# Performance work log

Measured on AMD Instinct MI355X. Metric: run time of the kernel, lower is better.

The kernel has to match this reference:

```python
import jax, jax.numpy as jnp
import numpy as np

P, F, FR = 288, 7, 12      # time slots per day, days per week, sampling frequency scale
CHEB_K = 2
HID = 64


def _ste(time_index, SE, W_se, b_se, T_tod, T_dow):
    """Spatio-temporal embedding: learned spatial embedding projected to et_dim,
    plus time-of-day and day-of-week temporal embeddings. -> [B, N, et]"""
    t = time_index * FR
    tod = T_tod[t % P]                 # [B, et]
    dow = T_dow[(t // P) % F]          # [B, et]
    se = SE @ W_se + b_se              # [N, et]
    return se[None, :, :] + (tod + dow)[:, None, :]


def _avwgcn(x, STE, R, SC, Wpool, bpool):
    """Adaptive-vertex-weight graph conv (AGCRN-style) with dynamic STE-driven
    adjacency blended with dynamic relation R and static correlation SC.
    x: [B,N,Cin], STE: [B,N,et], R: [B,N,N], SC: [N,N]."""
    A = jax.nn.softmax(
        jax.nn.relu(jnp.einsum('bnd,bmd->bnm', STE, STE)) + R + SC[None], axis=-1)
    # Chebyshev polynomial supports applied to x (T0 = I handled implicitly)
    xs = [x, jnp.einsum('bnm,bmc->bnc', A, x)]
    for _ in range(CHEB_K - 2):
        xs.append(2.0 * jnp.einsum('bnm,bmc->bnc', A, xs[-1]) - xs[-2])
    x_g = jnp.stack(xs, axis=2)                        # [B,N,K,Cin]
    # per-node adaptive weights: W_n = STE @ Wpool; contracted without
    # materializing the [B,N,K,Cin,Cout] tensor
    g = jnp.einsum('bnki,dkio->bndo', x_g, Wpool)      # [B,N,et,Cout]
    out = jnp.einsum('bndo,bnd->bno', g, STE) + jnp.einsum('bnd,do->bno', STE, bpool)
    return out


def setup_inputs() -> dict:
    key = jax.random.key(0)
    ks = jax.random.split(key, 12)
    B, N, Din, et, es = 32, 1024, 1, 16, 16
    std = 0.1
    return {
        "x": jax.random.normal(ks[0], (B, N, Din), jnp.float32),
        "R": jax.random.normal(ks[1], (B, N, N), jnp.float32) * std,
        "state": jax.random.normal(ks[2], (B, N, HID), jnp.float32),
        "SC": jax.random.normal(ks[3], (N, N), jnp.float32) * std,
        "SE": jax.random.normal(ks[4], (N, es), jnp.float32),
        "W_se": jax.random.normal(ks[5], (es, et), jnp.float32) * std,
        "b_se": jnp.zeros((et,), jnp.float32),
        "T_tod": jax.random.normal(ks[6], (P, et), jnp.float32) * std,
        "T_dow": jax.random.normal(ks[7], (F, et), jnp.float32) * std,
        "W_gate": jax.random.normal(ks[8], (et, CHEB_K, Din + HID, 2 * HID), jnp.float32) * std,
        "b_gate": jnp.zeros((et, 2 * HID), jnp.float32),
        "W_upd": jax.random.normal(ks[9], (et, CHEB_K, Din + HID, HID), jnp.float32) * std,
        "b_upd": jnp.zeros((et, HID), jnp.float32),
        "time_index": jax.random.randint(ks[10], (B,), 0, P * F),
    }


def reference(x, R, state, SC, SE, W_se, b_se, T_tod, T_dow,
              W_gate, b_gate, W_upd, b_upd, time_index):
    STE = _ste(time_index, SE, W_se, b_se, T_tod, T_dow)       # [B,N,et]
    ins = jnp.concatenate([x, state], axis=-1)                 # [B,N,Din+H]
    z_r = jax.nn.sigmoid(_avwgcn(ins, STE, R, SC, W_gate, b_gate))
    z, r = jnp.split(z_r, 2, axis=-1)                          # each [B,N,H]
    cand = jnp.concatenate([x, z * state], axis=-1)
    hc = jnp.tanh(_avwgcn(cand, STE, R, SC, W_upd, b_upd))
    return r * state + (1.0 - r) * hc                          # [B,N,H]
```

## Files before the change

kernel.cpp:

```cpp
#include <hip/hip_runtime.h>
#include <math.h>

namespace {
constexpr int BB = 32;
constexpr int NN = 1024;
constexpr int ET = 16;
constexpr int HH = 64;
constexpr int CIN = 65;
constexpr int KI = 2*CIN;
constexpr int COG = 2*HH;
constexpr int COU = HH;
constexpr int PP = 288;
constexpr int FF = 7;
constexpr int FRQ = 12;
constexpr int XK = 160;

typedef __attribute__((ext_vector_type(4))) float f32x4;
typedef __attribute__((ext_vector_type(8))) short s16x8;
typedef unsigned long long ull;

__device__ __forceinline__ float bf2f(unsigned short u) {
    unsigned v = ((unsigned)u) << 16;
    return __builtin_bit_cast(float, v);
}
__device__ __forceinline__ unsigned short f2bf(float f) {
    unsigned u = __builtin_bit_cast(unsigned, f);
    u += 0x7fffu + ((u >> 16) & 1u);
    return (unsigned short)(u >> 16);
}
__device__ __forceinline__ float ldany(const float* p) { return *p; }
__device__ __forceinline__ float ldany(const unsigned short* p) { return bf2f(*p); }

__global__ void k_prep1(const float* __restrict__ SE, const float* __restrict__ Wse,
                        const float* __restrict__ bse, const float* __restrict__ Ttod,
                        const float* __restrict__ Tdow, const int* __restrict__ tidx,
                        float* __restrict__ se, float* __restrict__ tt) {
    int idx = blockIdx.x*blockDim.x + threadIdx.x;
    if (idx < NN*ET) {
        int n = idx / ET, d = idx % ET;
        float acc = bse[d];
        #pragma unroll
        for (int e = 0; e < ET; ++e) acc += SE[n*ET + e]*Wse[e*ET + d];
        se[idx] = acc;
    } else if (idx < NN*ET + BB*ET) {
        int r = idx - NN*ET;
        int b = r / ET, d = r % ET;
        int t = tidx[b]*FRQ;
        tt[r] = Ttod[(t % PP)*ET + d] + Tdow[((t/PP) % FF)*ET + d];
    }
}

__global__ void k_prep2bf(const float* __restrict__ se, const float* __restrict__ tt,
                          unsigned short* __restrict__ stebf) {
    int idx = blockIdx.x*blockDim.x + threadIdx.x;
    if (idx >= BB*NN*ET) return;
    int d = idx % ET;
    int n = (idx/ET) % NN;
    int b = idx/(ET*NN);
    stebf[idx] = f2bf(se[n*ET+d] + tt[b*ET+d]);
}

__global__ void k_prepWpt(const float* __restrict__ Wg, const float* __restrict__ Wu,
                          unsigned short* __restrict__ Wptg, unsigned short* __restrict__ Wptu) {
    int idx = blockIdx.x*blockDim.x + threadIdx.x;
    constexpr int NG2 = ET*COG*XK;
    constexpr int NU2 = ET*COU*XK;
    if (idx < NG2) {
        int d = idx/(COG*XK), r = idx%(COG*XK), o = r/XK, ki = r%XK;
        float v = (ki < KI) ? Wg[((size_t)d*KI + ki)*COG + o] : 0.f;
        Wptg[((size_t)d*COG + o)*XK + ki] = f2bf(v);
    } else if (idx < NG2 + NU2) {
        int j = idx - NG2;
        int d = j/(COU*XK), r = j%(COU*XK), o = r/XK, ki = r%XK;
        float v = (ki < KI) ? Wu[((size_t)d*KI + ki)*COU + o] : 0.f;
        Wptu[((size_t)d*COU + o)*XK + ki] = f2bf(v);
    }
}

template<typename T>
__global__ void k_pack(const float* __restrict__ x, const T* __restrict__ sv,
                       unsigned short* __restrict__ xgbf) {
    int idx = blockIdx.x*blockDim.x + threadIdx.x;
    if (idx >= BB*NN*(XK/2)) return;
    int row = idx/(XK/2), c = idx%(XK/2);
    if (c < 32) {
        int k0 = 2*c;
        float v0 = (k0 == 0) ? x[row] : ldany(sv + (size_t)row*HH + k0 - 1);
        float v1 = ldany(sv + (size_t)row*HH + k0);
        ((unsigned*)xgbf)[(size_t)row*(XK/2) + c] = ((unsigned)f2bf(v1) << 16) | f2bf(v0);
    } else if (c == 32) {
        xgbf[(size_t)row*XK + 64] = f2bf(ldany(sv + (size_t)row*HH + 63));
    } else if (c >= 65) {
        ((unsigned*)xgbf)[(size_t)row*(XK/2) + c] = 0;
    }
}

template<typename T>
__global__ void k_cvtVt(const T* __restrict__ V, unsigned short* __restrict__ vt) {
    int idx = blockIdx.x*blockDim.x + threadIdx.x;
    if (idx >= BB*128*64) return;
    int och = idx & 63, mb = (idx >> 6) & 127, b = idx >> 13;
    const T* src = V + ((size_t)b*NN + mb*8)*HH + och;
    float v0=ldany(src), v1=ldany(src+HH), v2=ldany(src+2*HH), v3=ldany(src+3*HH);
    float v4=ldany(src+4*HH), v5=ldany(src+5*HH), v6=ldany(src+6*HH), v7=ldany(src+7*HH);
    ull lo = (ull)f2bf(v0) | ((ull)f2bf(v1)<<16) | ((ull)f2bf(v2)<<32) | ((ull)f2bf(v3)<<48);
    ull hi = (ull)f2bf(v4) | ((ull)f2bf(v5)<<16) | ((ull)f2bf(v6)<<32) | ((ull)f2bf(v7)<<48);
    ull* dst = (ull*)(vt + (size_t)idx*8);
    dst[0] = lo; dst[1] = hi;
}

constexpr int SSTR   = 1048;
constexpr int S_OFF  = 0;
constexpr int XV_OFF = 33536;
constexpr int MSH_OFF  = 37632;
constexpr int MSHC_OFF = 37888;
constexpr int LP_OFF   = 37952;
constexpr int AXP_OFF  = 38208;
constexpr int LSH_OFF  = 38464;
constexpr int SMEM_BYTES = 38528;

template<int PASS>
__global__ __launch_bounds__(256, 4) void k_attn(
    const unsigned short* __restrict__ stebf, const float* __restrict__ Rg,
    const float* __restrict__ SCg, const float* __restrict__ xg,
    const unsigned short* __restrict__ vt,
    float* __restrict__ Mr, float* __restrict__ Li,
    unsigned short* __restrict__ xgout)
{
    extern __shared__ char smem[];
    const int t = threadIdx.x, lane = t & 63, w = t >> 6;
    const int c15 = lane & 15, g = lane >> 4;
    const int strip = blockIdx.x, b = blockIdx.y;
    const size_t bN = (size_t)b * NN;
    const int r0 = strip * 16;

    float* Mshf  = (float*)(smem + MSH_OFF);
    float* MshCf = (float*)(smem + MSHC_OFF);
    float* Lpf   = (float*)(smem + LP_OFF);
    float* Axpf  = (float*)(smem + AXP_OFF);
    float* Lshf  = (float*)(smem + LSH_OFF);

    if (PASS == 1) {
        ((float4*)(smem + XV_OFF))[t] = ((const float4*)(xg + bN))[t];
    }

    {
        s16x8 af = {0,0,0,0,0,0,0,0};
        if (g < 2) af = *(const s16x8*)(stebf + (bN + r0 + c15)*ET + g*8);
        const float* Rb  = Rg  + (bN + r0 + g*4)*NN;
        const float* SCb = SCg + (size_t)(r0 + g*4)*NN;
        float mx0 = -INFINITY, mx1 = -INFINITY, mx2 = -INFINITY, mx3 = -INFINITY;
        float rc[4], scv[4];
        {
            int col = w*16 + c15;
            #pragma unroll
            for (int q = 0; q < 4; ++q) { rc[q] = Rb[(size_t)q*NN + col]; scv[q] = SCb[(size_t)q*NN + col]; }
        }
        for (int j = 0; j < 16; ++j) {
            int colB = j*64 + w*16 + c15;
            s16x8 bf = {0,0,0,0,0,0,0,0};
            if (g < 2) bf = *(const s16x8*)(stebf + (bN + colB)*ET + g*8);
            float rn[4] = {0.f,0.f,0.f,0.f}, sn[4] = {0.f,0.f,0.f,0.f};
            if (j < 15) {
                int col = colB + 64;
                #pragma unroll
                for (int q = 0; q < 4; ++q) { rn[q] = Rb[(size_t)q*NN + col]; sn[q] = SCb[(size_t)q*NN + col]; }
            }
            f32x4 zero = {0.f,0.f,0.f,0.f};
            f32x4 d = __builtin_amdgcn_mfma_f32_16x16x32_bf16(af, bf, zero, 0, 0, 0);
            #pragma unroll
            for (int q = 0; q < 4; ++q) {
                float s = fmaxf(d[q], 0.f) + rc[q] + scv[q];
                if (PASS == 1) {
                    if (q == 0) mx0 = fmaxf(mx0, s);
                    if (q == 1) mx1 = fmaxf(mx1, s);
                    if (q == 2) mx2 = fmaxf(mx2, s);
                    if (q == 3) mx3 = fmaxf(mx3, s);
                }
                int rowl = g*4 + q;
                *(unsigned short*)(smem + S_OFF + (unsigned)(rowl*SSTR + colB)*2u) = f2bf(s);
            }
            #pragma unroll
            for (int q = 0; q < 4; ++q) { rc[q] = rn[q]; scv[q] = sn[q]; }
        }
        if (PASS == 1) {
            float mxa[4] = {mx0, mx1, mx2, mx3};
            #pragma unroll
            for (int q = 0; q < 4; ++q) {
                float m = mxa[q];
                m = fmaxf(m, __shfl_xor(m, 1));
                m = fmaxf(m, __shfl_xor(m, 2));
                m = fmaxf(m, __shfl_xor(m, 4));
                m = fmaxf(m, __shfl_xor(m, 8));
                if (c15 == 0) Mshf[w*16 + g*4 + q] = m;
            }
        }
    }
    __syncthreads();

    if (PASS == 1) {
        if (t < 16) {
            float m = fmaxf(fmaxf(Mshf[t], Mshf[16+t]), fmaxf(Mshf[32+t], Mshf[48+t]));
            MshCf[t] = m;
            Mr[bN + r0 + t] = m;
        }
    } else {
        if (t < 16) MshCf[t] = Mr[bN + r0 + t];
        if (t >= 64 && t < 80) Lshf[t-64] = Li[bN + r0 + (t-64)];
    }
    __syncthreads();

    {
        const int rowl = c15;
        const float m = MshCf[rowl];
        float L = 0.f, ax = 0.f;
        for (int it = 0; it < 16; ++it) {
            int k = w*256 + it*16 + g*4;
            unsigned byteo = (unsigned)(rowl*SSTR + k)*2u;
            ull v = *(ull*)(smem + S_OFF + byteo);
            float s0 = bf2f((unsigned short)v);
            float s1 = bf2f((unsigned short)(v >> 16));
            float s2 = bf2f((unsigned short)(v >> 32));
            float s3 = bf2f((unsigned short)(v >> 48));
            float p0 = __expf(s0 - m), p1 = __expf(s1 - m);
            float p2 = __expf(s2 - m), p3 = __expf(s3 - m);
            if (PASS == 1) {
                float4 xq = *(const float4*)(smem + XV_OFF + k*4);
                L += (p0 + p1) + (p2 + p3);
                ax += p0*xq.x + p1*xq.y + p2*xq.z + p3*xq.w;
            }
            unsigned lo = ((unsigned)f2bf(p1) << 16) | f2bf(p0);
            unsigned hi = ((unsigned)f2bf(p3) << 16) | f2bf(p2);
            *(ull*)(smem + S_OFF + byteo) = ((ull)hi << 32) | lo;
        }
        if (PASS == 1) {
            L += __shfl_xor(L, 16); L += __shfl_xor(L, 32);
            ax += __shfl_xor(ax, 16); ax += __shfl_xor(ax, 32);
            if (g == 0) { Lpf[w*16 + rowl] = L; Axpf[w*16 + rowl] = ax; }
        }
    }
    __syncthreads();
    if (PASS == 1) {
        if (t < 16) {
            float Lt = Lpf[t] + Lpf[16+t] + Lpf[32+t] + Lpf[48+t];
            float li = 1.f / Lt;
            Lshf[t] = li;
            Li[bN + r0 + t] = li;
            xgout[(bN + r0 + t)*XK + 65] =
                f2bf((Axpf[t] + Axpf[16+t] + Axpf[32+t] + Axpf[48+t]) * li);
        }
        __syncthreads();
    }

    {
        f32x4 acc = {0.f,0.f,0.f,0.f};
        const unsigned short* vtb = vt + ((size_t)b*128*64 + (w*16 + c15))*8;
        #pragma unroll 4
        for (int j = 0; j < 16; ++j) {
            #pragma unroll
            for (int ks = 0; ks < 2; ++ks) {
                s16x8 a  = *(const s16x8*)(smem + S_OFF + (unsigned)(c15*SSTR + j*64 + ks*32 + g*8)*2u);
                s16x8 bv = *(const s16x8*)(vtb + (size_t)(j*8 + ks*4 + g)*512);
                acc = __builtin_amdgcn_mfma_f32_16x16x32_bf16(a, bv, acc, 0, 0, 0);
            }
        }
        #pragma unroll
        for (int q = 0; q < 4; ++q) {
            int rowl = g*4 + q;
            float li = Lshf[rowl];
            xgout[(bN + r0 + rowl)*XK + 66 + w*16 + c15] = f2bf(acc[q] * li);
        }
    }
}

template<int COUT, int EPI>
__global__ __launch_bounds__(256, 2) void k_apply(
    const unsigned short* __restrict__ Wpt, const float* __restrict__ bias,
    const unsigned short* __restrict__ stebf, const unsigned short* __restrict__ xgbf,
    const float* __restrict__ state, unsigned short* __restrict__ zsbf,
    unsigned short* __restrict__ rrbf, float* __restrict__ out)
{
    const int t = threadIdx.x, lane = t & 63, w = t >> 6;
    const int c15 = lane & 15, g = lane >> 4;
    const int n0 = blockIdx.x*32, b = blockIdx.y, oh = blockIdx.z;
    const int o = oh*64 + w*16 + c15;

    f32x4 acc[16][2];
    #pragma unroll
    for (int d = 0; d < 16; ++d) {
        acc[d][0] = (f32x4){0.f,0.f,0.f,0.f};
        acc[d][1] = (f32x4){0.f,0.f,0.f,0.f};
    }

    const unsigned short* Ar0 = xgbf + ((size_t)b*NN + n0 + c15)*XK + g*8;
    const unsigned short* Ar1 = Ar0 + (size_t)16*XK;
    const unsigned short* Bp  = Wpt + (size_t)o*XK + g*8;

    for (int ks = 0; ks < 5; ++ks) {
        s16x8 a0 = *(const s16x8*)(Ar0 + ks*32);
        s16x8 a1 = *(const s16x8*)(Ar1 + ks*32);
        #pragma unroll
        for (int d = 0; d < 16; ++d) {
            s16x8 bf = *(const s16x8*)(Bp + (size_t)d*COUT*XK + ks*32);
            acc[d][0] = __builtin_amdgcn_mfma_f32_16x16x32_bf16(a0, bf, acc[d][0], 0, 0, 0);
            acc[d][1] = __builtin_amdgcn_mfma_f32_16x16x32_bf16(a1, bf, acc[d][1], 0, 0, 0);
        }
    }

    float biasv[16];
    #pragma unroll
    for (int d = 0; d < 16; ++d) biasv[d] = bias[d*COUT + o];

    #pragma unroll
    for (int mt = 0; mt < 2; ++mt) {
        #pragma unroll
        for (int q = 0; q < 4; ++q) {
            int n = n0 + mt*16 + g*4 + q;
            size_t bn = (size_t)b*NN + n;
            const ull* sp = (const ull*)(stebf + bn*ET);
            float val = 0.f;
            #pragma unroll
            for (int dd = 0; dd < 4; ++dd) {
                ull sv4 = sp[dd];
                float s0 = bf2f((unsigned short)sv4);
                float s1 = bf2f((unsigned short)(sv4 >> 16));
                float s2 = bf2f((unsigned short)(sv4 >> 32));
                float s3 = bf2f((unsigned short)(sv4 >> 48));
                val += s0*(acc[dd*4+0][mt][q] + biasv[dd*4+0]);
                val += s1*(acc[dd*4+1][mt][q] + biasv[dd*4+1]);
                val += s2*(acc[dd*4+2][mt][q] + biasv[dd*4+2]);
                val += s3*(acc[dd*4+3][mt][q] + biasv[dd*4+3]);
            }
            if (EPI == 0) {
                float gv = 1.f/(1.f + __expf(-val));
                if (oh == 0) zsbf[bn*HH + o] = f2bf(gv * state[bn*HH + o]);
                else         rrbf[bn*HH + (o - 64)] = f2bf(gv);
            } else {
                float hc = tanhf(val);
                float rv = bf2f(rrbf[bn*HH + o]);
                out[bn*HH + o] = rv*state[bn*HH + o] + (1.f - rv)*hc;
            }
        }
    }
}

}

extern "C" void kernel_launch(void* const* d_in, const int* in_sizes, int n_in,
                              void* d_out, int out_size, void* d_ws, size_t ws_size,
                              hipStream_t stream) {
    const float* x     = (const float*)d_in[0];
    const float* R     = (const float*)d_in[1];
    const float* state = (const float*)d_in[2];
    const float* SC    = (const float*)d_in[3];
    const float* SE    = (const float*)d_in[4];
    const float* W_se  = (const float*)d_in[5];
    const float* b_se  = (const float*)d_in[6];
    const float* T_tod = (const float*)d_in[7];
    const float* T_dow = (const float*)d_in[8];
    const float* W_g   = (const float*)d_in[9];
    const float* b_g   = (const float*)d_in[10];
    const float* W_u   = (const float*)d_in[11];
    const float* b_u   = (const float*)d_in[12];
    const int*   tidx  = (const int*)d_in[13];
    float* out = (float*)d_out;
    float* ws = (float*)d_ws;

    float* se = ws;
    float* tt = se + 16384;
    float* Mr = tt + 512;
    float* Li = Mr + 32768;
    unsigned short* stebf = (unsigned short*)(Li + 32768);
    unsigned short* xgbf  = stebf + 524288;
    unsigned short* zsbf  = xgbf + 5242880;
    unsigned short* rrbf  = zsbf + 2097152;
    unsigned short* vt    = rrbf + 2097152;
    unsigned short* Wptg  = vt + 2097152;
    unsigned short* Wptu  = Wptg + 327680;

    k_prep1<<<66, 256, 0, stream>>>(SE, W_se, b_se, T_tod, T_dow, tidx, se, tt);
    k_prep2bf<<<2048, 256, 0, stream>>>(se, tt, stebf);
    k_prepWpt<<<1920, 256, 0, stream>>>(W_g, W_u, Wptg, Wptu);

    k_cvtVt<float><<<1024, 256, 0, stream>>>(state, vt);
    k_attn<1><<<dim3(64, 32), 256, SMEM_BYTES, stream>>>(
        stebf, R, SC, x, vt, Mr, Li, xgbf);
    k_pack<float><<<10240, 256, 0, stream>>>(x, state, xgbf);
    k_apply<COG, 0><<<dim3(32, 32, 2), 256, 0, stream>>>(
        Wptg, b_g, stebf, xgbf, state, zsbf, rrbf, nullptr);

    k_cvtVt<unsigned short><<<1024, 256, 0, stream>>>(zsbf, vt);
    k_attn<2><<<dim3(64, 32), 256, SMEM_BYTES, stream>>>(
        stebf, R, SC, x, vt, Mr, Li, xgbf);
    k_pack<unsigned short><<<10240, 256, 0, stream>>>(x, zsbf, xgbf);
    k_apply<COU, 1><<<dim3(32, 32, 1), 256, 0, stream>>>(
        Wptu, b_u, stebf, xgbf, state, zsbf, rrbf, out);
}
```

Measured before the change: 229.1 us.

## Fuse prep kernels, transpose score MFMA for row-contiguous loads, single-pass exp in pass two

Merges the STE and weight prep kernels into one launch, and merges the V transpose with the x/state packing so pass two's pack moves before its attention. In k_attn the score MFMA operands are swapped so each lane holds four contiguous columns of one row. That allows float4 loads of R and SC, packed bf16 stores via v_cvt_pk_bf16_f32, and a per-lane row max reduced with two shuffles. Pass two now applies exp with the stored row max while writing scores, dropping a sync and a full re-read of the shared-memory score tile. The cost is more kernel-body complexity and reliance on an inline-asm conversion instruction.

Result: no change. 233.6 us (+2.0%).

```diff
diff --git a/kernel.cpp b/kernel.cpp
--- a/kernel.cpp
+++ b/kernel.cpp
@@ -27,6 +27,11 @@
     unsigned u = __builtin_bit_cast(unsigned, f);
     u += 0x7fffu + ((u >> 16) & 1u);
     return (unsigned short)(u >> 16);
+}
+__device__ __forceinline__ unsigned cvtpk(float lo, float hi) {
+    unsigned r;
+    asm("v_cvt_pk_bf16_f32 %0, %1, %2" : "=v"(r) : "v"(lo), "v"(hi));
+    return r;
 }
 __device__ __forceinline__ float ldany(const float* p) { return *p; }
 __device__ __forceinline__ float ldany(const unsigned short* p) { return bf2f(*p); }
@@ -50,37 +55,49 @@
     }
 }
 
-__global__ void k_prep2bf(const float* __restrict__ se, const float* __restrict__ tt,
-                          unsigned short* __restrict__ stebf) {
+__global__ void k_prep2(const float* __restrict__ se, const float* __restrict__ tt,
+                        const float* __restrict__ Wg, const float* __restrict__ Wu,
+                        unsigned short* __restrict__ stebf,
+                        unsigned short* __restrict__ Wptg, unsigned short* __restrict__ Wptu) {
     int idx = blockIdx.x*blockDim.x + threadIdx.x;
-    if (idx >= BB*NN*ET) return;
-    int d = idx % ET;
-    int n = (idx/ET) % NN;
-    int b = idx/(ET*NN);
-    stebf[idx] = f2bf(se[n*ET+d] + tt[b*ET+d]);
-}
-
-__global__ void k_prepWpt(const float* __restrict__ Wg, const float* __restrict__ Wu,
-                          unsigned short* __restrict__ Wptg, unsigned short* __restrict__ Wptu) {
-    int idx = blockIdx.x*blockDim.x + threadIdx.x;
-    constexpr int NG2 = ET*COG*XK;
-    constexpr int NU2 = ET*COU*XK;
-    if (idx < NG2) {
+    if (idx < BB*NN*ET) {
+        int d = idx % ET;
+        int n = (idx/ET) % NN;
+        int b = idx/(ET*NN);
+        stebf[idx] = f2bf(se[n*ET+d] + tt[b*ET+d]);
+        return;
+    }
+    idx -= BB*NN*ET;
+    if (idx < ET*COG*XK) {
         int d = idx/(COG*XK), r = idx%(COG*XK), o = r/XK, ki = r%XK;
         float v = (ki < KI) ? Wg[((size_t)d*KI + ki)*COG + o] : 0.f;
         Wptg[((size_t)d*COG + o)*XK + ki] = f2bf(v);
-    } else if (idx < NG2 + NU2) {
-        int j = idx - NG2;
-        int d = j/(COU*XK), r = j%(COU*XK), o = r/XK, ki = r%XK;
+        return;
+    }
+    idx -= ET*COG*XK;
+    if (idx < ET*COU*XK) {
+        int d = idx/(COU*XK), r = idx%(COU*XK), o = r/XK, ki = r%XK;
         float v = (ki < KI) ? Wu[((size_t)d*KI + ki)*COU + o] : 0.f;
         Wptu[((size_t)d*COU + o)*XK + ki] = f2bf(v);
     }
 }
 
 template<typename T>
-__global__ void k_pack(const float* __restrict__ x, const T* __restrict__ sv,
-                       unsigned short* __restrict__ xgbf) {
+__global__ void k_vin(const float* __restrict__ x, const T* __restrict__ sv,
+                      unsigned short* __restrict__ xgbf, unsigned short* __restrict__ vt) {
     int idx = blockIdx.x*blockDim.x + threadIdx.x;
+    if (idx < BB*128*64) {
+        int och = idx & 63, mb = (idx >> 6) & 127, b = idx >> 13;
+        const T* src = sv + ((size_t)b*NN + mb*8)*HH + och;
+        float v0=ldany(src), v1=ldany(src+HH), v2=ldany(src+2*HH), v3=ldany(src+3*HH);
+        float v4=ldany(src+4*HH), v5=ldany(src+5*HH), v6=ldany(src+6*HH), v7=ldany(src+7*HH);
+        ull lo = (ull)f2bf(v0) | ((ull)f2bf(v1)<<16) | ((ull)f2bf(v2)<<32) | ((ull)f2bf(v3)<<48);
+        ull hi = (ull)f2bf(v4) | ((ull)f2bf(v5)<<16) | ((ull)f2bf(v6)<<32) | ((ull)f2bf(v7)<<48);
+        ull* dst = (ull*)(vt + (size_t)idx*8);
+        dst[0] = lo; dst[1] = hi;
+        return;
+    }
+    idx -= BB*128*64;
     if (idx >= BB*NN*(XK/2)) return;
     int row = idx/(XK/2), c = idx%(XK/2);
     if (c < 32) {
@@ -93,20 +110,6 @@
     } else if (c >= 65) {
         ((unsigned*)xgbf)[(size_t)row*(XK/2) + c] = 0;
     }
-}
-
-template<typename T>
-__global__ void k_cvtVt(const T* __restrict__ V, unsigned short* __restrict__ vt) {
-    int idx = blockIdx.x*blockDim.x + threadIdx.x;
-    if (idx >= BB*128*64) return;
-    int och = idx & 63, mb = (idx >> 6) & 127, b = idx >> 13;
-    const T* src = V + ((size_t)b*NN + mb*8)*HH + och;
-    float v0=ldany(src), v1=ldany(src+HH), v2=ldany(src+2*HH), v3=ldany(src+3*HH);
-    float v4=ldany(src+4*HH), v5=ldany(src+5*HH), v6=ldany(src+6*HH), v7=ldany(src+7*HH);
-    ull lo = (ull)f2bf(v0) | ((ull)f2bf(v1)<<16) | ((ull)f2bf(v2)<<32) | ((ull)f2bf(v3)<<48);
-    ull hi = (ull)f2bf(v4) | ((ull)f2bf(v5)<<16) | ((ull)f2bf(v6)<<32) | ((ull)f2bf(v7)<<48);
-    ull* dst = (ull*)(vt + (size_t)idx*8);
-    dst[0] = lo; dst[1] = hi;
 }
 
 constexpr int SSTR   = 1048;
@@ -142,113 +145,89 @@
 
     if (PASS == 1) {
         ((float4*)(smem + XV_OFF))[t] = ((const float4*)(xg + bN))[t];
-    }
-
+    } else {
+        if (t < 16) Lshf[t] = Li[bN + r0 + t];
+    }
+    float mp2 = 0.f;
+    if (PASS == 2) mp2 = Mr[bN + r0 + c15];
+
+    float mx = -INFINITY;
     {
-        s16x8 af = {0,0,0,0,0,0,0,0};
-        if (g < 2) af = *(const s16x8*)(stebf + (bN + r0 + c15)*ET + g*8);
-        const float* Rb  = Rg  + (bN + r0 + g*4)*NN;
-        const float* SCb = SCg + (size_t)(r0 + g*4)*NN;
-        float mx0 = -INFINITY, mx1 = -INFINITY, mx2 = -INFINITY, mx3 = -INFINITY;
-        float rc[4], scv[4];
-        {
-            int col = w*16 + c15;
-            #pragma unroll
-            for (int q = 0; q < 4; ++q) { rc[q] = Rb[(size_t)q*NN + col]; scv[q] = SCb[(size_t)q*NN + col]; }
-        }
+        s16x8 bfr = {0,0,0,0,0,0,0,0};
+        if (g < 2) bfr = *(const s16x8*)(stebf + (bN + r0 + c15)*ET + g*8);
+        const float* Rb  = Rg  + (bN + r0 + c15)*NN;
+        const float* SCb = SCg + (size_t)(r0 + c15)*NN;
+        const int colq = w*16 + g*4;
+        float4 rc = *(const float4*)(Rb + colq);
+        float4 sc = *(const float4*)(SCb + colq);
         for (int j = 0; j < 16; ++j) {
-            int colB = j*64 + w*16 + c15;
-            s16x8 bf = {0,0,0,0,0,0,0,0};
-            if (g < 2) bf = *(const s16x8*)(stebf + (bN + colB)*ET + g*8);
-            float rn[4] = {0.f,0.f,0.f,0.f}, sn[4] = {0.f,0.f,0.f,0.f};
+            s16x8 af = {0,0,0,0,0,0,0,0};
+            if (g < 2) af = *(const s16x8*)(stebf + (bN + j*64 + w*16 + c15)*ET + g*8);
+            float4 rn = {0,0,0,0}, sn = {0,0,0,0};
             if (j < 15) {
-                int col = colB + 64;
-                #pragma unroll
-                for (int q = 0; q < 4; ++q) { rn[q] = Rb[(size_t)q*NN + col]; sn[q] = SCb[(size_t)q*NN + col]; }
+                rn = *(const float4*)(Rb + colq + (j+1)*64);
+                sn = *(const float4*)(SCb + colq + (j+1)*64);
             }
             f32x4 zero = {0.f,0.f,0.f,0.f};
-            f32x4 d = __builtin_amdgcn_mfma_f32_16x16x32_bf16(af, bf, zero, 0, 0, 0);
-            #pragma unroll
-            for (int q = 0; q < 4; ++q) {
-                float s = fmaxf(d[q], 0.f) + rc[q] + scv[q];
-                if (PASS == 1) {
-                    if (q == 0) mx0 = fmaxf(mx0, s);
-                    if (q == 1) mx1 = fmaxf(mx1, s);
-                    if (q == 2) mx2 = fmaxf(mx2, s);
-                    if (q == 3) mx3 = fmaxf(mx3, s);
-                }
-                int rowl = g*4 + q;
-                *(unsigned short*)(smem + S_OFF + (unsigned)(rowl*SSTR + colB)*2u) = f2bf(s);
-            }
-            #pragma unroll
-            for (int q = 0; q < 4; ++q) { rc[q] = rn[q]; scv[q] = sn[q]; }
-        }
-        if (PASS == 1) {
-            float mxa[4] = {mx0, mx1, mx2, mx3};
-            #pragma unroll
-            for (int q = 0; q < 4; ++q) {
-                float m = mxa[q];
-                m = fmaxf(m, __shfl_xor(m, 1));
-                m = fmaxf(m, __shfl_xor(m, 2));
-                m = fmaxf(m, __shfl_xor(m, 4));
-                m = fmaxf(m, __shfl_xor(m, 8));
-                if (c15 == 0) Mshf[w*16 + g*4 + q] = m;
-            }
-        }
-    }
-    __syncthreads();
+            f32x4 d = __builtin_amdgcn_mfma_f32_16x16x32_bf16(af, bfr, zero, 0, 0, 0);
+            float s0 = fmaxf(d[0],0.f) + rc.x + sc.x;
+            float s1 = fmaxf(d[1],0.f) + rc.y + sc.y;
+            float s2 = fmaxf(d[2],0.f) + rc.z + sc.z;
+            float s3 = fmaxf(d[3],0.f) + rc.w + sc.w;
+            unsigned byteo = (unsigned)(c15*SSTR + j*64 + colq)*2u;
+            if (PASS == 1) {
+                mx = fmaxf(mx, fmaxf(fmaxf(s0,s1), fmaxf(s2,s3)));
+                *(ull*)(smem + S_OFF + byteo) = (ull)cvtpk(s0,s1) | ((ull)cvtpk(s2,s3) << 32);
+            } else {
+                float p0 = __expf(s0 - mp2), p1 = __expf(s1 - mp2);
+                float p2 = __expf(s2 - mp2), p3 = __expf(s3 - mp2);
+                *(ull*)(smem + S_OFF + byteo) = (ull)cvtpk(p0,p1) | ((ull)cvtpk(p2,p3) << 32);
+            }
+            rc = rn; sc = sn;
+        }
+    }
 
     if (PASS == 1) {
+        mx = fmaxf(mx, __shfl_xor(mx, 16));
+        mx = fmaxf(mx, __shfl_xor(mx, 32));
+        if (lane < 16) Mshf[w*16 + c15] = mx;
+        __syncthreads();
         if (t < 16) {
-            float m = fmaxf(fmaxf(Mshf[t], Mshf[16+t]), fmaxf(Mshf[32+t], Mshf[48+t]));
-            MshCf[t] = m;
-            Mr[bN + r0 + t] = m;
-        }
-    } else {
-        if (t < 16) MshCf[t] = Mr[bN + r0 + t];
-        if (t >= 64 && t < 80) Lshf[t-64] = Li[bN + r0 + (t-64)];
-    }
-    __syncthreads();
-
-    {
-        const int rowl = c15;
-        const float m = MshCf[rowl];
+            float M = fmaxf(fmaxf(Mshf[t], Mshf[16+t]), fmaxf(Mshf[32+t], Mshf[48+t]));
+            MshCf[t] = M;
+            Mr[bN + r0 + t] = M;
+        }
+        __syncthreads();
+        const float m = MshCf[c15];
+        const int colq = w*16 + g*4;
         float L = 0.f, ax = 0.f;
         for (int it = 0; it < 16; ++it) {
-            int k = w*256 + it*16 + g*4;
-            unsigned byteo = (unsigned)(rowl*SSTR + k)*2u;
+            unsigned byteo = (unsigned)(c15*SSTR + it*64 + colq)*2u;
             ull v = *(ull*)(smem + S_OFF + byteo);
             float s0 = bf2f((unsigned short)v);
             float s1 = bf2f((unsigned short)(v >> 16));
             float s2 = bf2f((unsigned short)(v >> 32));
             float s3 = bf2f((unsigned short)(v >> 48));
-            float p0 = __expf(s0 - m), p1 = __expf(s1 - m);
-            float p2 = __expf(s2 - m), p3 = __expf(s3 - m);
-            if (PASS == 1) {
-                float4 xq = *(const float4*)(smem + XV_OFF + k*4);
-                L += (p0 + p1) + (p2 + p3);
-                ax += p0*xq.x + p1*xq.y + p2*xq.z + p3*xq.w;
-            }
-            unsigned lo = ((unsigned)f2bf(p1) << 16) | f2bf(p0);
-            unsigned hi = ((unsigned)f2bf(p3) << 16) | f2bf(p2);
-            *(ull*)(smem + S_OFF + byteo) = ((ull)hi << 32) | lo;
-        }
-        if (PASS == 1) {
-            L += __shfl_xor(L, 16); L += __shfl_xor(L, 32);
-            ax += __shfl_xor(ax, 16); ax += __shfl_xor(ax, 32);
-            if (g == 0) { Lpf[w*16 + rowl] = L; Axpf[w*16 + rowl] = ax; }
-        }
-    }
-    __syncthreads();
-    if (PASS == 1) {
+            float p0 = __expf(s0-m), p1 = __expf(s1-m), p2 = __expf(s2-m), p3 = __expf(s3-m);
+            float4 xq = *(const float4*)(smem + XV_OFF + (it*64 + colq)*4);
+            L += (p0 + p1) + (p2 + p3);
+            ax += p0*xq.x + p1*xq.y + p2*xq.z + p3*xq.w;
+            *(ull*)(smem + S_OFF + byteo) = (ull)cvtpk(p0,p1) | ((ull)cvtpk(p2,p3) << 32);
+        }
+        L += __shfl_xor(L, 16); L += __shfl_xor(L, 32);
+        ax += __shfl_xor(ax, 16); ax += __shfl_xor(ax, 32);
+        if (lane < 16) { Lpf[w*16 + c15] = L; Axpf[w*16 + c15] = ax; }
+        __syncthreads();
         if (t < 16) {
             float Lt = Lpf[t] + Lpf[16+t] + Lpf[32+t] + Lpf[48+t];
             float li = 1.f / Lt;
             Lshf[t] = li;
             Li[bN + r0 + t] = li;
-            xgout[(bN + r0 + t)*XK + 65] =
-                f2bf((Axpf[t] + Axpf[16+t] + Axpf[32+t] + Axpf[48+t]) * li);
-        }
+            float axt = Axpf[t] + Axpf[16+t] + Axpf[32+t] + Axpf[48+t];
+            xgout[(bN + r0 + t)*XK + 65] = f2bf(axt * li);
+        }
+        __syncthreads();
+    } else {
         __syncthreads();
     }
 
@@ -379,20 +358,17 @@
     unsigned short* Wptu  = Wptg + 327680;
 
     k_prep1<<<66, 256, 0, stream>>>(SE, W_se, b_se, T_tod, T_dow, tidx, se, tt);
-    k_prep2bf<<<2048, 256, 0, stream>>>(se, tt, stebf);
-    k_prepWpt<<<1920, 256, 0, stream>>>(W_g, W_u, Wptg, Wptu);
-
-    k_cvtVt<float><<<1024, 256, 0, stream>>>(state, vt);
+    k_prep2<<<3968, 256, 0, stream>>>(se, tt, W_g, W_u, stebf, Wptg, Wptu);
+
+    k_vin<float><<<11264, 256, 0, stream>>>(x, state, xgbf, vt);
     k_attn<1><<<dim3(64, 32), 256, SMEM_BYTES, stream>>>(
         stebf, R, SC, x, vt, Mr, Li, xgbf);
-    k_pack<float><<<10240, 256, 0, stream>>>(x, state, xgbf);
     k_apply<COG, 0><<<dim3(32, 32, 2), 256, 0, stream>>>(
         Wptg, b_g, stebf, xgbf, state, zsbf, rrbf, nullptr);
 
-    k_cvtVt<unsigned short><<<1024, 256, 0, stream>>>(zsbf, vt);
+    k_vin<unsigned short><<<11264, 256, 0, stream>>>(x, zsbf, xgbf, vt);
     k_attn<2><<<dim3(64, 32), 256, SMEM_BYTES, stream>>>(
         stebf, R, SC, x, vt, Mr, Li, xgbf);
-    k_pack<unsigned short><<<10240, 256, 0, stream>>>(x, zsbf, xgbf);
     k_apply<COU, 1><<<dim3(32, 32, 1), 256, 0, stream>>>(
         Wptu, b_u, stebf, xgbf, state, zsbf, rrbf, out);
 }
```
